# Performance work log

Hardware: AMD Instinct MI355X
Metric: run time of the kernel (lower is better)

The kernel has to match this reference:

```python
import jax, jax.numpy as jnp
import numpy as np

N, INC, INN, OUTC, OUTN, MAXD = 8, 64, 20000, 64, 8000, 32


def setup_inputs() -> dict:
    key = jax.random.key(0)
    k0, k1, k2, k3, k4 = jax.random.split(key, 5)
    # adjacency list: outn nodes, degree in [8, 32], padded to MAXD with index 0
    rng = np.random.default_rng(0)
    deg = rng.integers(8, MAXD + 1, size=OUTN)                      # (outn,)
    A_np = rng.integers(0, INN, size=(OUTN, MAXD))                  # (outn, maxD)
    valid = np.arange(MAXD)[None, :] < deg[:, None]
    A_np = np.where(valid, A_np, 0)
    # '_norm' option: mask entries are 1/degree for valid slots, 0 for pad
    mask_np = valid.astype(np.float32) / deg[:, None].astype(np.float32)

    x = jax.random.normal(k0, (N, INC, INN), dtype=jnp.float32)
    # hadamard weight: sqrt(2/inn) * U(-1, 1)
    weight = np.sqrt(2.0 / INN).astype(np.float32) * (
        2.0 * jax.random.uniform(k1, (INC, INN), dtype=jnp.float32) - 1.0)
    # weight_norm Linear(inc, outc): v (outc, inc) direction, g (outc,) magnitude
    ct_v = jax.random.normal(k2, (OUTC, INC), dtype=jnp.float32) * (1.0 / np.sqrt(INC).astype(np.float32))
    ct_g = 0.5 + jax.random.uniform(k3, (OUTC,), dtype=jnp.float32)
    bias = 0.2 * jax.random.normal(k4, (1, OUTC, OUTN), dtype=jnp.float32)
    return {
        'x': x,
        'weight': weight,
        'ct_v': ct_v,
        'ct_g': ct_g,
        'bias': bias,
        'mask': jnp.asarray(mask_np),
        'A': jnp.asarray(A_np, dtype=jnp.int32),
    }


def reference(x, weight, ct_v, ct_g, bias, mask, A):
    # x: (N, inc, inn); weight: (inc, inn)
    xw = x * weight                                   # hadamard
    gathered = xw[:, :, A]                            # (N, inc, outn, maxD) adjacency gather
    pooled = jnp.einsum('bcod,od->bco', gathered, mask)  # degree-normalized masked sum
    # weight_norm: W = g * v / ||v||_row
    W = ct_g[:, None] * ct_v / jnp.linalg.norm(ct_v, axis=1, keepdims=True)  # (outc, inc)
    y = jnp.einsum('bco,kc->bko', pooled, W)          # (N, outc, outn)
    return y + bias
```

## Files before the change

kernel.cpp:

```cpp
#include <hip/hip_runtime.h>
#include <stdint.h>

#define NB   8
#define INC  64
#define INN  20000
#define OUTC 64
#define OUTN 8000
#define MAXD 32

typedef float f32x2 __attribute__((ext_vector_type(2)));

__global__ void prep_kernel(const int* __restrict__ A, const float* __restrict__ mask,
                            const float* __restrict__ ct_v, const float* __restrict__ ct_g,
                            uint4* __restrict__ AQ, float2* __restrict__ scale2,
                            float* __restrict__ W_T) {
    if (blockIdx.x == 64) {
        int k = threadIdx.x;
        if (k < OUTC) {
            float s = 0.f;
            for (int c = 0; c < INC; ++c) { float v = ct_v[k * INC + c]; s += v * v; }
            float inv = ct_g[k] / sqrtf(s);
            for (int c = 0; c < INC; ++c) W_T[c * OUTC + k] = ct_v[k * INC + c] * inv;
        }
        return;
    }
    int o = blockIdx.x * 128 + threadIdx.x;
    if (o >= OUTN) return;
    const int4* arow = (const int4*)(A + (size_t)o * MAXD);
#pragma unroll
    for (int j = 0; j < 4; ++j) {
        int4 v0 = arow[2 * j];
        int4 v1 = arow[2 * j + 1];
        uint4 pk;
        pk.x = (uint32_t)(v0.x << 1) | ((uint32_t)(v0.y << 1) << 16);
        pk.y = (uint32_t)(v0.z << 1) | ((uint32_t)(v0.w << 1) << 16);
        pk.z = (uint32_t)(v1.x << 1) | ((uint32_t)(v1.y << 1) << 16);
        pk.w = (uint32_t)(v1.z << 1) | ((uint32_t)(v1.w << 1) << 16);
        AQ[(size_t)j * OUTN + o] = pk;
    }
    float invdeg = mask[(size_t)o * MAXD];
    float deg    = rintf(1.0f / invdeg);
    scale2[o] = make_float2(invdeg * (1.0f / 256.0f), 32.0f - deg);
}

__global__ __launch_bounds__(256)
void xw_kernel(const float* __restrict__ x, const float* __restrict__ w,
               uint32_t* __restrict__ xwi) {
    int t    = threadIdx.x;
    int tile = blockIdx.x;
    int g    = blockIdx.y;
    int b    = blockIdx.z;
    int i0   = tile * 1024 + t * 4;
    if (i0 >= INN) return;
    int c0 = g * 4;
    const float* xb = x + ((size_t)b * INC + c0) * INN + i0;
    const float* wb = w + (size_t)c0 * INN + i0;
    float4 p[4];
#pragma unroll
    for (int cl = 0; cl < 4; ++cl) {
        float4 xv = *(const float4*)(xb + (size_t)cl * INN);
        float4 wv = *(const float4*)(wb + (size_t)cl * INN);
        p[cl] = make_float4(xv.x * wv.x * 256.0f, xv.y * wv.y * 256.0f,
                            xv.z * wv.z * 256.0f, xv.w * wv.w * 256.0f);
    }
    uint4 out;
    {
        uint32_t u;
        u = __builtin_amdgcn_cvt_pk_fp8_f32(p[0].x, p[1].x, 0, false);
        u = __builtin_amdgcn_cvt_pk_fp8_f32(p[2].x, p[3].x, u, true);
        out.x = u;
        u = __builtin_amdgcn_cvt_pk_fp8_f32(p[0].y, p[1].y, 0, false);
        u = __builtin_amdgcn_cvt_pk_fp8_f32(p[2].y, p[3].y, u, true);
        out.y = u;
        u = __builtin_amdgcn_cvt_pk_fp8_f32(p[0].z, p[1].z, 0, false);
        u = __builtin_amdgcn_cvt_pk_fp8_f32(p[2].z, p[3].z, u, true);
        out.z = u;
        u = __builtin_amdgcn_cvt_pk_fp8_f32(p[0].w, p[1].w, 0, false);
        u = __builtin_amdgcn_cvt_pk_fp8_f32(p[2].w, p[3].w, u, true);
        out.w = u;
    }
    *(uint4*)(xwi + ((size_t)(b * 16 + g)) * INN + i0) = out;
}

__global__ __launch_bounds__(1024, 8)
void gather_kernel(const uint32_t* __restrict__ xwi, const uint4* __restrict__ AQ,
                   const float2* __restrict__ scale2, float* __restrict__ pooled) {
    __shared__ __align__(16) uint32_t smem[INN];
    int s  = blockIdx.x;
    int g  = blockIdx.y;
    int b  = blockIdx.z;
    int tid = threadIdx.x;
    int c0 = g * 4;

    const uint4* src = (const uint4*)(xwi + ((size_t)(b * 16 + g)) * INN);
#pragma unroll
    for (int k = 0; k < 5; ++k) {
        int i = tid + k * 1024;
        if (i < INN / 4) {
            __builtin_amdgcn_global_load_lds(
                (const __attribute__((address_space(1))) uint32_t*)(src + i),
                (__attribute__((address_space(3))) uint32_t*)((char*)smem + ((i & ~63) * 16)),
                16, 0, 0);
        }
    }

    int obase = s * 1000;
    int o     = obase + tid;
    int oc    = (tid < 1000) ? o : obase;
    uint4 q0 = AQ[oc];
    uint4 q1 = AQ[OUTN + oc];
    uint4 q2 = AQ[2 * OUTN + oc];
    uint4 q3 = AQ[3 * OUTN + oc];
    float2 sc = scale2[oc];

    __syncthreads();

    uint32_t zw = smem[0];
    f32x2 ze0 = __builtin_amdgcn_cvt_pk_f32_fp8(zw, false);
    f32x2 ze1 = __builtin_amdgcn_cvt_pk_f32_fp8(zw, true);

    const char* sb = (const char*)smem;
    float a0 = 0.f, a1 = 0.f, a2 = 0.f, a3 = 0.f;

#define DO_U32(u)                                                   \
    {                                                               \
        uint32_t off0 = (u & 0xFFFFu) << 1;                         \
        uint32_t off1 = (u >> 16) << 1;                             \
        uint32_t v0 = *(const uint32_t*)(sb + off0);                \
        uint32_t v1 = *(const uint32_t*)(sb + off1);                \
        f32x2 e;                                                    \
        e = __builtin_amdgcn_cvt_pk_f32_fp8(v0, false);             \
        a0 += e.x; a1 += e.y;                                       \
        e = __builtin_amdgcn_cvt_pk_f32_fp8(v0, true);              \
        a2 += e.x; a3 += e.y;                                       \
        e = __builtin_amdgcn_cvt_pk_f32_fp8(v1, false);             \
        a0 += e.x; a1 += e.y;                                       \
        e = __builtin_amdgcn_cvt_pk_f32_fp8(v1, true);              \
        a2 += e.x; a3 += e.y;                                       \
    }
    DO_U32(q0.x) DO_U32(q0.y) DO_U32(q0.z) DO_U32(q0.w)
    DO_U32(q1.x) DO_U32(q1.y) DO_U32(q1.z) DO_U32(q1.w)
    DO_U32(q2.x) DO_U32(q2.y) DO_U32(q2.z) DO_U32(q2.w)
    DO_U32(q3.x) DO_U32(q3.y) DO_U32(q3.z) DO_U32(q3.w)
#undef DO_U32

    if (tid < 1000) {
        float r0 = (a0 - sc.y * ze0.x) * sc.x;
        float r1 = (a1 - sc.y * ze0.y) * sc.x;
        float r2 = (a2 - sc.y * ze1.x) * sc.x;
        float r3 = (a3 - sc.y * ze1.y) * sc.x;
        pooled[((size_t)(b * OUTC + c0 + 0)) * OUTN + o] = r0;
        pooled[((size_t)(b * OUTC + c0 + 1)) * OUTN + o] = r1;
        pooled[((size_t)(b * OUTC + c0 + 2)) * OUTN + o] = r2;
        pooled[((size_t)(b * OUTC + c0 + 3)) * OUTN + o] = r3;
    }
}

__global__ __launch_bounds__(256)
void out_kernel(float* io, const float* __restrict__ W_T,
                const float* __restrict__ bias) {
    __shared__ __align__(16) float sp[INC][128];
    __shared__ __align__(16) float sw[INC][OUTC];
    int obase = blockIdx.x * 128;
    int b     = blockIdx.y;

    const float* pb = io + (size_t)b * INC * OUTN;
    for (int idx = threadIdx.x; idx < INC * 32; idx += 256) {
        int c  = idx >> 5;
        int q  = idx & 31;
        int o4 = obase + q * 4;
        float4 v = (o4 < OUTN) ? *(const float4*)(pb + (size_t)c * OUTN + o4)
                               : make_float4(0.f, 0.f, 0.f, 0.f);
        *(float4*)(&sp[c][q * 4]) = v;
    }
    for (int idx = threadIdx.x; idx < (INC * OUTC) / 4; idx += 256) {
        ((float4*)sw)[idx] = ((const float4*)W_T)[idx];
    }
    __syncthreads();

    int t   = threadIdx.x;
    int kt  = t >> 4;
    int ot0 = (t & 15) * 8;
    int k0  = kt * 4;

    float acc[4][8];
#pragma unroll
    for (int kk = 0; kk < 4; ++kk) {
#pragma unroll
        for (int jh = 0; jh < 2; ++jh) {
            int o4 = obase + ot0 + jh * 4;
            float4 bv = (o4 < OUTN)
                ? *(const float4*)(bias + (size_t)(k0 + kk) * OUTN + o4)
                : make_float4(0.f, 0.f, 0.f, 0.f);
            acc[kk][jh * 4 + 0] = bv.x;
            acc[kk][jh * 4 + 1] = bv.y;
            acc[kk][jh * 4 + 2] = bv.z;
            acc[kk][jh * 4 + 3] = bv.w;
        }
    }

#pragma unroll 4
    for (int c = 0; c < INC; ++c) {
        float4 w4  = *(const float4*)(&sw[c][k0]);
        float4 pa  = *(const float4*)(&sp[c][ot0]);
        float4 pb4 = *(const float4*)(&sp[c][ot0 + 4]);
        float p[8] = {pa.x, pa.y, pa.z, pa.w, pb4.x, pb4.y, pb4.z, pb4.w};
        float wv[4] = {w4.x, w4.y, w4.z, w4.w};
#pragma unroll
        for (int kk = 0; kk < 4; ++kk)
#pragma unroll
            for (int j = 0; j < 8; ++j)
                acc[kk][j] += wv[kk] * p[j];
    }

    int o0 = obase + ot0;
    if (o0 < OUTN) {
#pragma unroll
        for (int kk = 0; kk < 4; ++kk) {
            float4 s0 = make_float4(acc[kk][0], acc[kk][1], acc[kk][2], acc[kk][3]);
            float4 s1 = make_float4(acc[kk][4], acc[kk][5], acc[kk][6], acc[kk][7]);
            float* dst = io + ((size_t)(b * OUTC + k0 + kk)) * OUTN + o0;
            *(float4*)(dst)     = s0;
            *(float4*)(dst + 4) = s1;
        }
    }
}

extern "C" void kernel_launch(void* const* d_in, const int* in_sizes, int n_in,
                              void* d_out, int out_size, void* d_ws, size_t ws_size,
                              hipStream_t stream) {
    const float* x    = (const float*)d_in[0];
    const float* w    = (const float*)d_in[1];
    const float* ct_v = (const float*)d_in[2];
    const float* ct_g = (const float*)d_in[3];
    const float* bias = (const float*)d_in[4];
    const float* mask = (const float*)d_in[5];
    const int*   A    = (const int*)d_in[6];
    float* y = (float*)d_out;

    char* ws = (char*)d_ws;
    uint32_t* xwi    = (uint32_t*)(ws);
    uint4*    AQ     = (uint4*)(ws + 10240000);
    float2*   scale2 = (float2*)(ws + 10752000);
    float*    W_T    = (float*)(ws + 10816000);

    xw_kernel<<<dim3(20, 16, NB), 256, 0, stream>>>(x, w, xwi);
    prep_kernel<<<65, 128, 0, stream>>>(A, mask, ct_v, ct_g, AQ, scale2, W_T);
    gather_kernel<<<dim3(8, 16, NB), 1024, 0, stream>>>(xwi, AQ, scale2, y);
    out_kernel<<<dim3(63, NB), 256, 0, stream>>>(y, W_T, bias);
}
```

Baseline: 52.57 us.

## Fuse prep into xw kernel and double-buffer channel groups in gather

```diff
diff --git a/kernel.cpp b/kernel.cpp
--- a/kernel.cpp
+++ b/kernel.cpp
@@ -10,43 +10,45 @@
 
 typedef float f32x2 __attribute__((ext_vector_type(2)));
 
-__global__ void prep_kernel(const int* __restrict__ A, const float* __restrict__ mask,
-                            const float* __restrict__ ct_v, const float* __restrict__ ct_g,
-                            uint4* __restrict__ AQ, float2* __restrict__ scale2,
-                            float* __restrict__ W_T) {
-    if (blockIdx.x == 64) {
-        int k = threadIdx.x;
-        if (k < OUTC) {
-            float s = 0.f;
-            for (int c = 0; c < INC; ++c) { float v = ct_v[k * INC + c]; s += v * v; }
-            float inv = ct_g[k] / sqrtf(s);
-            for (int c = 0; c < INC; ++c) W_T[c * OUTC + k] = ct_v[k * INC + c] * inv;
-        }
+__global__ __launch_bounds__(256)
+void xw_prep_kernel(const float* __restrict__ x, const float* __restrict__ w,
+                    const int* __restrict__ A, const float* __restrict__ mask,
+                    const float* __restrict__ ct_v, const float* __restrict__ ct_g,
+                    uint32_t* __restrict__ xwi, uint4* __restrict__ AQ,
+                    float2* __restrict__ scale2, float* __restrict__ W_T) {
+    int t = threadIdx.x;
+    if (blockIdx.z == 8) {
+        int flat = blockIdx.y * 20 + blockIdx.x;
+        if (flat == 63) {
+            int k = t;
+            if (k < OUTC) {
+                float s = 0.f;
+                for (int c = 0; c < INC; ++c) { float v = ct_v[k * INC + c]; s += v * v; }
+                float inv = ct_g[k] / sqrtf(s);
+                for (int c = 0; c < INC; ++c) W_T[c * OUTC + k] = ct_v[k * INC + c] * inv;
+            }
+            return;
+        }
+        if (flat > 63 || t >= 128) return;
+        int o = flat * 128 + t;
+        if (o >= OUTN) return;
+        const int4* arow = (const int4*)(A + (size_t)o * MAXD);
+#pragma unroll
+        for (int j = 0; j < 4; ++j) {
+            int4 v0 = arow[2 * j];
+            int4 v1 = arow[2 * j + 1];
+            uint4 pk;
+            pk.x = (uint32_t)(v0.x << 1) | ((uint32_t)(v0.y << 1) << 16);
+            pk.y = (uint32_t)(v0.z << 1) | ((uint32_t)(v0.w << 1) << 16);
+            pk.z = (uint32_t)(v1.x << 1) | ((uint32_t)(v1.y << 1) << 16);
+            pk.w = (uint32_t)(v1.z << 1) | ((uint32_t)(v1.w << 1) << 16);
+            AQ[(size_t)j * OUTN + o] = pk;
+        }
+        float invdeg = mask[(size_t)o * MAXD];
+        float deg    = rintf(1.0f / invdeg);
+        scale2[o] = make_float2(invdeg * (1.0f / 256.0f), 32.0f - deg);
         return;
     }
-    int o = blockIdx.x * 128 + threadIdx.x;
-    if (o >= OUTN) return;
-    const int4* arow = (const int4*)(A + (size_t)o * MAXD);
-#pragma unroll
-    for (int j = 0; j < 4; ++j) {
-        int4 v0 = arow[2 * j];
-        int4 v1 = arow[2 * j + 1];
-        uint4 pk;
-        pk.x = (uint32_t)(v0.x << 1) | ((uint32_t)(v0.y << 1) << 16);
-        pk.y = (uint32_t)(v0.z << 1) | ((uint32_t)(v0.w << 1) << 16);
-        pk.z = (uint32_t)(v1.x << 1) | ((uint32_t)(v1.y << 1) << 16);
-        pk.w = (uint32_t)(v1.z << 1) | ((uint32_t)(v1.w << 1) << 16);
-        AQ[(size_t)j * OUTN + o] = pk;
-    }
-    float invdeg = mask[(size_t)o * MAXD];
-    float deg    = rintf(1.0f / invdeg);
-    scale2[o] = make_float2(invdeg * (1.0f / 256.0f), 32.0f - deg);
-}
-
-__global__ __launch_bounds__(256)
-void xw_kernel(const float* __restrict__ x, const float* __restrict__ w,
-               uint32_t* __restrict__ xwi) {
-    int t    = threadIdx.x;
     int tile = blockIdx.x;
     int g    = blockIdx.y;
     int b    = blockIdx.z;
@@ -82,27 +84,33 @@
     *(uint4*)(xwi + ((size_t)(b * 16 + g)) * INN + i0) = out;
 }
 
-__global__ __launch_bounds__(1024, 8)
+__global__ __launch_bounds__(1024, 4)
 void gather_kernel(const uint32_t* __restrict__ xwi, const uint4* __restrict__ AQ,
                    const float2* __restrict__ scale2, float* __restrict__ pooled) {
-    __shared__ __align__(16) uint32_t smem[INN];
+    __shared__ __align__(16) uint32_t smem[2][INN];
     int s  = blockIdx.x;
-    int g  = blockIdx.y;
+    int gy = blockIdx.y;
     int b  = blockIdx.z;
     int tid = threadIdx.x;
-    int c0 = g * 4;
-
-    const uint4* src = (const uint4*)(xwi + ((size_t)(b * 16 + g)) * INN);
-#pragma unroll
-    for (int k = 0; k < 5; ++k) {
-        int i = tid + k * 1024;
-        if (i < INN / 4) {
-            __builtin_amdgcn_global_load_lds(
-                (const __attribute__((address_space(1))) uint32_t*)(src + i),
-                (__attribute__((address_space(3))) uint32_t*)((char*)smem + ((i & ~63) * 16)),
-                16, 0, 0);
-        }
-    }
+
+    int g0 = gy * 4;
+    const uint32_t* tab = xwi + (size_t)b * 16 * INN;
+
+#define DMA(gq, buf)                                                            \
+    {                                                                           \
+        const uint4* srcq = (const uint4*)(tab + (size_t)(gq) * INN);           \
+        _Pragma("unroll")                                                       \
+        for (int k = 0; k < 5; ++k) {                                           \
+            int i = tid + k * 1024;                                             \
+            if (i < INN / 4) {                                                  \
+                __builtin_amdgcn_global_load_lds(                               \
+                    (const __attribute__((address_space(1))) uint32_t*)(srcq + i), \
+                    (__attribute__((address_space(3))) uint32_t*)((char*)smem[buf] + ((i & ~63) * 16)), \
+                    16, 0, 0);                                                  \
+            }                                                                   \
+        }                                                                       \
+    }
+    DMA(g0, 0)
 
     int obase = s * 1000;
     int o     = obase + tid;
@@ -112,48 +120,57 @@
     uint4 q2 = AQ[2 * OUTN + oc];
     uint4 q3 = AQ[3 * OUTN + oc];
     float2 sc = scale2[oc];
+    bool active = (tid < 1000);
 
     __syncthreads();
 
-    uint32_t zw = smem[0];
-    f32x2 ze0 = __builtin_amdgcn_cvt_pk_f32_fp8(zw, false);
-    f32x2 ze1 = __builtin_amdgcn_cvt_pk_f32_fp8(zw, true);
-
-    const char* sb = (const char*)smem;
-    float a0 = 0.f, a1 = 0.f, a2 = 0.f, a3 = 0.f;
-
+#pragma unroll
+    for (int j = 0; j < 4; ++j) {
+        int cur = j & 1;
+        if (j < 3) DMA(g0 + j + 1, (j + 1) & 1)
+
+        uint32_t zw = smem[cur][0];
+        f32x2 ze0 = __builtin_amdgcn_cvt_pk_f32_fp8(zw, false);
+        f32x2 ze1 = __builtin_amdgcn_cvt_pk_f32_fp8(zw, true);
+
+        const char* sb = (const char*)smem[cur];
+        float a0 = 0.f, a1 = 0.f, a2 = 0.f, a3 = 0.f;
 #define DO_U32(u)                                                   \
-    {                                                               \
-        uint32_t off0 = (u & 0xFFFFu) << 1;                         \
-        uint32_t off1 = (u >> 16) << 1;                             \
-        uint32_t v0 = *(const uint32_t*)(sb + off0);                \
-        uint32_t v1 = *(const uint32_t*)(sb + off1);                \
-        f32x2 e;                                                    \
-        e = __builtin_amdgcn_cvt_pk_f32_fp8(v0, false);             \
-        a0 += e.x; a1 += e.y;                                       \
-        e = __builtin_amdgcn_cvt_pk_f32_fp8(v0, true);              \
-        a2 += e.x; a3 += e.y;                                       \
-        e = __builtin_amdgcn_cvt_pk_f32_fp8(v1, false);             \
-        a0 += e.x; a1 += e.y;                                       \
-        e = __builtin_amdgcn_cvt_pk_f32_fp8(v1, true);              \
-        a2 += e.x; a3 += e.y;                                       \
-    }
-    DO_U32(q0.x) DO_U32(q0.y) DO_U32(q0.z) DO_U32(q0.w)
-    DO_U32(q1.x) DO_U32(q1.y) DO_U32(q1.z) DO_U32(q1.w)
-    DO_U32(q2.x) DO_U32(q2.y) DO_U32(q2.z) DO_U32(q2.w)
-    DO_U32(q3.x) DO_U32(q3.y) DO_U32(q3.z) DO_U32(q3.w)
+        {                                                           \
+            uint32_t off0 = (u & 0xFFFFu) << 1;                     \
+            uint32_t off1 = (u >> 16) << 1;                         \
+            uint32_t v0 = *(const uint32_t*)(sb + off0);            \
+            uint32_t v1 = *(const uint32_t*)(sb + off1);            \
+            f32x2 e;                                                \
+            e = __builtin_amdgcn_cvt_pk_f32_fp8(v0, false);         \
+            a0 += e.x; a1 += e.y;                                   \
+            e = __builtin_amdgcn_cvt_pk_f32_fp8(v0, true);          \
+            a2 += e.x; a3 += e.y;                                   \
+            e = __builtin_amdgcn_cvt_pk_f32_fp8(v1, false);         \
+            a0 += e.x; a1 += e.y;                                   \
+            e = __builtin_amdgcn_cvt_pk_f32_fp8(v1, true);          \
+            a2 += e.x; a3 += e.y;                                   \
+        }
+        DO_U32(q0.x) DO_U32(q0.y) DO_U32(q0.z) DO_U32(q0.w)
+        DO_U32(q1.x) DO_U32(q1.y) DO_U32(q1.z) DO_U32(q1.w)
+        DO_U32(q2.x) DO_U32(q2.y) DO_U32(q2.z) DO_U32(q2.w)
+        DO_U32(q3.x) DO_U32(q3.y) DO_U32(q3.z) DO_U32(q3.w)
 #undef DO_U32
 
-    if (tid < 1000) {
-        float r0 = (a0 - sc.y * ze0.x) * sc.x;
-        float r1 = (a1 - sc.y * ze0.y) * sc.x;
-        float r2 = (a2 - sc.y * ze1.x) * sc.x;
-        float r3 = (a3 - sc.y * ze1.y) * sc.x;
-        pooled[((size_t)(b * OUTC + c0 + 0)) * OUTN + o] = r0;
-        pooled[((size_t)(b * OUTC + c0 + 1)) * OUTN + o] = r1;
-        pooled[((size_t)(b * OUTC + c0 + 2)) * OUTN + o] = r2;
-        pooled[((size_t)(b * OUTC + c0 + 3)) * OUTN + o] = r3;
-    }
+        if (active) {
+            int c0 = (g0 + j) * 4;
+            float r0 = (a0 - sc.y * ze0.x) * sc.x;
+            float r1 = (a1 - sc.y * ze0.y) * sc.x;
+            float r2 = (a2 - sc.y * ze1.x) * sc.x;
+            float r3 = (a3 - sc.y * ze1.y) * sc.x;
+            pooled[((size_t)(b * OUTC + c0 + 0)) * OUTN + o] = r0;
+            pooled[((size_t)(b * OUTC + c0 + 1)) * OUTN + o] = r1;
+            pooled[((size_t)(b * OUTC + c0 + 2)) * OUTN + o] = r2;
+            pooled[((size_t)(b * OUTC + c0 + 3)) * OUTN + o] = r3;
+        }
+        __syncthreads();
+    }
+#undef DMA
 }
 
 __global__ __launch_bounds__(256)
@@ -244,8 +261,8 @@
     float2*   scale2 = (float2*)(ws + 10752000);
     float*    W_T    = (float*)(ws + 10816000);
 
-    xw_kernel<<<dim3(20, 16, NB), 256, 0, stream>>>(x, w, xwi);
-    prep_kernel<<<65, 128, 0, stream>>>(A, mask, ct_v, ct_g, AQ, scale2, W_T);
-    gather_kernel<<<dim3(8, 16, NB), 1024, 0, stream>>>(xwi, AQ, scale2, y);
+    xw_prep_kernel<<<dim3(20, 16, 9), 256, 0, stream>>>(x, w, A, mask, ct_v, ct_g,
+                                                        xwi, AQ, scale2, W_T);
+    gather_kernel<<<dim3(8, 4, NB), 1024, 0, stream>>>(xwi, AQ, scale2, y);
     out_kernel<<<dim3(63, NB), 256, 0, stream>>>(y, W_T, bias);
 }
```

After: 51.04 us. 1.03x faster.
